# Kernel optimization log

Measured on AMD Instinct MI355X. Metric: run time of the kernel, lower is better.

Reference implementation:

```python
import jax, jax.numpy as jnp
import numpy as np

NUM_ITER = 3
HEADS = 8
EPS = 1e-8

def _ln(x, g, b, eps=1e-5):
    mu = x.mean(-1, keepdims=True)
    var = ((x - mu) ** 2).mean(-1, keepdims=True)
    return (x - mu) * jax.lax.rsqrt(var + eps) * g + b

def setup_inputs() -> dict:
    key = jax.random.key(0)
    ks = jax.random.split(key, 10)
    B, Nkv, Din = 32, 4096, 256
    Nq, S, Hm = 16, 256, 512
    def xav(k, shape):
        lim = (6.0 / (shape[0] + shape[1])) ** 0.5
        return jax.random.uniform(k, shape, minval=-lim, maxval=lim, dtype=jnp.float32)
    return {
        "slots": jax.random.normal(ks[0], (Nq, S), dtype=jnp.float32),
        "inputs": jax.random.normal(ks[1], (B, Nkv, Din), dtype=jnp.float32),
        "norm_in_g": jnp.ones((Din,), jnp.float32), "norm_in_b": jnp.zeros((Din,), jnp.float32),
        "norm_slots_g": jnp.ones((S,), jnp.float32), "norm_slots_b": jnp.zeros((S,), jnp.float32),
        "norm_mlp_g": jnp.ones((S,), jnp.float32), "norm_mlp_b": jnp.zeros((S,), jnp.float32),
        "Wq": xav(ks[2], (S, S)), "Wk": xav(ks[3], (S, Din)), "Wv": xav(ks[4], (S, Din)),
        "gru_wih": xav(ks[5], (3 * S, S)),
        "gru_whh": jax.random.normal(ks[6], (3 * S, S), dtype=jnp.float32) * (1.0 / S ** 0.5),
        "gru_bih": jnp.zeros((3 * S,), jnp.float32), "gru_bhh": jnp.zeros((3 * S,), jnp.float32),
        "mlp_w1": xav(ks[7], (Hm, S)), "mlp_b1": jnp.zeros((Hm,), jnp.float32),
        "mlp_w2": xav(ks[8], (S, Hm)), "mlp_b2": jnp.zeros((S,), jnp.float32),
    }

def reference(slots, inputs, norm_in_g, norm_in_b, norm_slots_g, norm_slots_b,
              norm_mlp_g, norm_mlp_b, Wq, Wk, Wv, gru_wih, gru_whh, gru_bih, gru_bhh,
              mlp_w1, mlp_b1, mlp_w2, mlp_b2):
    B, Nkv, Din = inputs.shape
    Nq, S = slots.shape
    H = HEADS
    hd = S // H
    slots = jnp.broadcast_to(slots, (B, Nq, S))
    x = _ln(inputs, norm_in_g, norm_in_b)
    k = (x @ Wk.T).reshape(B, Nkv, H, hd).transpose(0, 2, 1, 3) * (hd ** -0.5)  # [B,H,Nkv,hd]
    v = (x @ Wv.T).reshape(B, Nkv, H, hd).transpose(0, 2, 1, 3)
    attn_vis = None
    for _ in range(NUM_ITER):
        slots_prev = slots
        s = _ln(slots, norm_slots_g, norm_slots_b)
        q = (s @ Wq.T).reshape(B, Nq, H, hd).transpose(0, 2, 1, 3)  # [B,H,Nq,hd]
        # logits [B,Nkv,H*Nq]; softmax jointly over heads and slots per key (slot-axis softmax)
        logits = jnp.einsum('bhkd,bhqd->bkhq', k, q).reshape(B, Nkv, H * Nq)
        attn = jax.nn.softmax(logits, axis=-1).reshape(B, Nkv, H, Nq).transpose(0, 2, 1, 3)  # [B,H,Nkv,Nq]
        attn_vis = attn.sum(1)  # [B,Nkv,Nq]
        attn_n = attn / (attn.sum(axis=2, keepdims=True) + EPS)  # normalize over keys
        updates = jnp.einsum('bhkq,bhkd->bqhd', attn_n, v).reshape(B, Nq, S)
        # GRUCell: gates order r,z,n
        xg = updates.reshape(-1, S)
        h = slots_prev.reshape(-1, S)
        gi = xg @ gru_wih.T + gru_bih
        gh = h @ gru_whh.T + gru_bhh
        ir, iz, inn = jnp.split(gi, 3, axis=-1)
        hr, hz, hn = jnp.split(gh, 3, axis=-1)
        r = jax.nn.sigmoid(ir + hr)
        z = jax.nn.sigmoid(iz + hz)
        n = jnp.tanh(inn + r * hn)
        slots = ((1.0 - z) * n + z * h).reshape(B, Nq, S)
        m = _ln(slots, norm_mlp_g, norm_mlp_b)
        slots = slots + (jax.nn.relu(m @ mlp_w1.T + mlp_b1) @ mlp_w2.T + mlp_b2)
    return (slots, attn_vis)
```

## Files before the change

### kernel.cpp

```cpp
#include <hip/hip_runtime.h>
#include <stdint.h>

typedef unsigned short u16;
typedef __attribute__((ext_vector_type(8))) _Float16 half8;
typedef __attribute__((ext_vector_type(4))) _Float16 half4;
typedef __attribute__((ext_vector_type(4))) float floatx4;

__device__ inline float bflo(unsigned u){ return __uint_as_float(u << 16); }
__device__ inline float bfhi(unsigned u){ return __uint_as_float(u & 0xffff0000u); }
__device__ inline float bf1(u16 v){ return __uint_as_float(((unsigned)v) << 16); }
__device__ inline u16 f2bf(float f){
  unsigned u = __float_as_uint(f);
  u += 0x7fffu + ((u >> 16) & 1u);
  return (u16)(u >> 16);
}
__device__ inline float dot8(uint4 w, float4 a, float4 b, float acc){
  acc = fmaf(bflo(w.x), a.x, acc); acc = fmaf(bfhi(w.x), a.y, acc);
  acc = fmaf(bflo(w.y), a.z, acc); acc = fmaf(bfhi(w.y), a.w, acc);
  acc = fmaf(bflo(w.z), b.x, acc); acc = fmaf(bfhi(w.z), b.y, acc);
  acc = fmaf(bflo(w.w), b.z, acc); acc = fmaf(bfhi(w.w), b.w, acc);
  return acc;
}

#define CW_SLOTS 0
#define CW_GIN   4096
#define CW_BIN   4352
#define CW_GS    4608
#define CW_BS    4864
#define CW_GM    5120
#define CW_BM    5376
#define CW_WQ    5632
#define CW_WK    71168
#define CW_WV    136704
#define CW_WIH   202240
#define CW_WHH   398848
#define CW_BIH   595456
#define CW_BHH   596224
#define CW_W1    596992
#define CW_B1    728064
#define CW_W2    728576
#define CW_B2    859648
#define CW_TOTAL 859904

__global__ void k_flag(const u16* __restrict__ probe, int* __restrict__ flag){
  int t = threadIdx.x;
  int bad = 0;
  #pragma unroll
  for (int i = 0; i < 4; i++){
    float x = bf1(probe[t + i * 256]);
    if (!(fabsf(x) < 1e6f)) bad = 1;
  }
  __shared__ int s;
  if (t == 0) s = 0;
  __syncthreads();
  if (bad) atomicOr(&s, 1);
  __syncthreads();
  if (t == 0) *flag = s;
}

struct CanonArgs { const void* p[18]; };

__global__ void k_canon(CanonArgs a, const int* __restrict__ flag, u16* __restrict__ cw){
  const int off[19] = {CW_SLOTS, CW_GIN, CW_BIN, CW_GS, CW_BS, CW_GM, CW_BM, CW_WQ,
                       CW_WK, CW_WV, CW_WIH, CW_WHH, CW_BIH, CW_BHH, CW_W1, CW_B1,
                       CW_W2, CW_B2, CW_TOTAL};
  int i = blockIdx.x * 256 + threadIdx.x;
  if (i >= CW_TOTAL) return;
  int f32m = *flag;
  int j = 0;
  while (i >= off[j + 1]) j++;
  int local = i - off[j];
  float v = f32m ? ((const float*)a.p[j])[local] : bf1(((const u16*)a.p[j])[local]);
  cw[i] = f2bf(v);
}

__global__ void k_init(const u16* __restrict__ cw, float* __restrict__ slots,
                       _Float16* __restrict__ wkvh)
{
  int idx = blockIdx.x * 256 + threadIdx.x;
  if (idx < 131072){
    float g = bf1(cw[CW_GIN + (idx & 255)]);
    wkvh[idx] = (_Float16)(bf1(cw[CW_WK + idx]) * g);
  } else {
    int i = idx - 131072;
    int d = i & 255;
    int q = (i >> 8) & 15;
    slots[i] = bf1(cw[CW_SLOTS + q * 256 + d]);
  }
}

__global__ void k_beta(const u16* __restrict__ cw, float* __restrict__ beta){
  int c = blockIdx.x * 256 + threadIdx.x;
  if (c >= 512) return;
  float a = 0.f;
  for (int d = 0; d < 256; d++)
    a = fmaf(bf1(cw[CW_BIN + d]), bf1(cw[CW_WK + c * 256 + d]), a);
  beta[c] = a;
}

__global__ __launch_bounds__(256) void k0_stats(
    const void* __restrict__ inp, const int* __restrict__ flag, float2* __restrict__ stats)
{
  int f32m = *flag;
  int g = blockIdx.x * 256 + threadIdx.x;
  int row = g >> 4, l = g & 15;
  float sum = 0.f, sq = 0.f;
  if (f32m){
    const float* rp = (const float*)inp + row * 256 + l * 16;
    #pragma unroll
    for (int i = 0; i < 4; i++){
      float4 v = ((const float4*)rp)[i];
      sum += v.x + v.y + v.z + v.w;
      sq = fmaf(v.x, v.x, sq); sq = fmaf(v.y, v.y, sq);
      sq = fmaf(v.z, v.z, sq); sq = fmaf(v.w, v.w, sq);
    }
  } else {
    const u16* rp = (const u16*)inp + row * 256 + l * 16;
    #pragma unroll
    for (int i = 0; i < 2; i++){
      uint4 u = ((const uint4*)rp)[i];
      unsigned w[4] = {u.x, u.y, u.z, u.w};
      #pragma unroll
      for (int p = 0; p < 4; p++){
        float a = bflo(w[p]), b = bfhi(w[p]);
        sum += a + b; sq = fmaf(a, a, sq); sq = fmaf(b, b, sq);
      }
    }
  }
  #pragma unroll
  for (int m = 1; m < 16; m <<= 1){ sum += __shfl_xor(sum, m); sq += __shfl_xor(sq, m); }
  if (l == 0){
    float mu = sum * (1.f/256.f);
    float var = sq * (1.f/256.f) - mu * mu;
    stats[row] = make_float2(mu, rsqrtf(var + 1e-5f));
  }
}

__global__ __launch_bounds__(256) void k1_gemm(
    const void* __restrict__ inp, const int* __restrict__ flag,
    const float2* __restrict__ stats, const float* __restrict__ beta,
    const _Float16* __restrict__ wkvh, _Float16* __restrict__ kh, _Float16* __restrict__ vT)
{
  int f32m = *flag;
  int tid = threadIdx.x;
  int wv = tid >> 6, lane = tid & 63;
  int m16 = lane & 15, q4 = lane >> 4;
  int nb = blockIdx.y;
  long rowb0 = (long)blockIdx.x * 128;
  int colW = nb * 256 + wv * 64;

  half8 bfr[4][8];
  #pragma unroll
  for (int nt = 0; nt < 4; nt++)
    #pragma unroll
    for (int s = 0; s < 8; s++)
      bfr[nt][s] = *(const half8*)(wkvh + (colW + nt * 16 + m16) * 256 + s * 32 + q4 * 8);

  float bet[4];
  #pragma unroll
  for (int nt = 0; nt < 4; nt++) bet[nt] = beta[colW + nt * 16 + m16];

  for (int rt = 0; rt < 8; rt++){
    long rowb = rowb0 + rt * 16;
    long myRow = rowb + m16;
    float2 st = stats[myRow];
    float mu = st.x, rstd = st.y;

    half8 af[8];
    if (f32m){
      const float* rp = (const float*)inp + myRow * 256 + q4 * 8;
      #pragma unroll
      for (int s = 0; s < 8; s++){
        float4 x0 = *(const float4*)(rp + s * 32);
        float4 x1 = *(const float4*)(rp + s * 32 + 4);
        af[s][0] = (_Float16)((x0.x - mu) * rstd); af[s][1] = (_Float16)((x0.y - mu) * rstd);
        af[s][2] = (_Float16)((x0.z - mu) * rstd); af[s][3] = (_Float16)((x0.w - mu) * rstd);
        af[s][4] = (_Float16)((x1.x - mu) * rstd); af[s][5] = (_Float16)((x1.y - mu) * rstd);
        af[s][6] = (_Float16)((x1.z - mu) * rstd); af[s][7] = (_Float16)((x1.w - mu) * rstd);
      }
    } else {
      const u16* rp = (const u16*)inp + myRow * 256 + q4 * 8;
      #pragma unroll
      for (int s = 0; s < 8; s++){
        uint4 xu = *(const uint4*)(rp + s * 32);
        unsigned xw[4] = {xu.x, xu.y, xu.z, xu.w};
        #pragma unroll
        for (int p = 0; p < 4; p++){
          af[s][2*p]   = (_Float16)((bflo(xw[p]) - mu) * rstd);
          af[s][2*p+1] = (_Float16)((bfhi(xw[p]) - mu) * rstd);
        }
      }
    }

    floatx4 acc[4];
    #pragma unroll
    for (int nt = 0; nt < 4; nt++){
      acc[nt][0] = bet[nt]; acc[nt][1] = bet[nt]; acc[nt][2] = bet[nt]; acc[nt][3] = bet[nt];
    }
    #pragma unroll
    for (int s = 0; s < 8; s++)
      #pragma unroll
      for (int nt = 0; nt < 4; nt++)
        acc[nt] = __builtin_amdgcn_mfma_f32_16x16x32_f16(af[s], bfr[nt][s], acc[nt], 0, 0, 0);

    if (nb == 0){
      long crow = rowb + q4 * 4;
      #pragma unroll
      for (int nt = 0; nt < 4; nt++)
        #pragma unroll
        for (int r = 0; r < 4; r++)
          kh[(crow + r) * 256 + colW + nt * 16 + m16] = (_Float16)acc[nt][r];
    } else {
      int b = (int)(rowb >> 12);
      int key = ((int)rowb & 4095) + q4 * 4;
      int kg  = key >> 6;
      int klo = key & 63;
      #pragma unroll
      for (int nt = 0; nt < 4; nt++){
        int cv = (colW - 256) + nt * 16 + m16;
        half4 pk;
        pk[0] = (_Float16)acc[nt][0]; pk[1] = (_Float16)acc[nt][1];
        pk[2] = (_Float16)acc[nt][2]; pk[3] = (_Float16)acc[nt][3];
        *(half4*)(vT + (((long)b * 64 + kg) * 256 + cv) * 64 + klo) = pk;
      }
    }
  }
}

__global__ __launch_bounds__(256) void k2_q(
    const float* __restrict__ slots, const u16* __restrict__ cw, _Float16* __restrict__ qh,
    float* __restrict__ denom, float* __restrict__ numer, int lastIter)
{
  const u16* gq = cw + CW_GS;
  const u16* bq = cw + CW_BS;
  const u16* Wq = cw + CW_WQ;
  int row = blockIdx.x, tid = threadIdx.x;
  if (lastIter) numer[row * 256 + tid] = 0.f;
  if (row < 16) denom[row * 256 + tid] = 0.f;
  int wv = tid >> 6, lane = tid & 63;
  float x = slots[row * 256 + tid];
  float s = x, s2 = x * x;
  #pragma unroll
  for (int m = 1; m < 64; m <<= 1){ s += __shfl_xor(s, m); s2 += __shfl_xor(s2, m); }
  __shared__ float red[8];
  if (lane == 0){ red[wv] = s; red[4 + wv] = s2; }
  __syncthreads();
  float tot  = red[0] + red[1] + red[2] + red[3];
  float tot2 = red[4] + red[5] + red[6] + red[7];
  float mu = tot * (1.f/256.f);
  float rstd = rsqrtf(tot2 * (1.f/256.f) - mu * mu + 1e-5f);
  __shared__ float sln[256];
  sln[tid] = (x - mu) * rstd * bf1(gq[tid]) + bf1(bq[tid]);
  __syncthreads();
  const u16* wr = Wq + tid * 256;
  float a = 0.f;
  for (int k = 0; k < 256; k += 8){
    uint4 wu = *(const uint4*)(wr + k);
    float4 l0 = *(const float4*)(sln + k);
    float4 l1 = *(const float4*)(sln + k + 4);
    a = dot8(wu, l0, l1, a);
  }
  qh[row * 256 + tid] = (_Float16)(a * 0.17677669529663687f);
}

__global__ __launch_bounds__(256) void k3_attn(
    const _Float16* __restrict__ kh, const _Float16* __restrict__ vT,
    const _Float16* __restrict__ qh,
    float* __restrict__ denom, float* __restrict__ numer,
    void* __restrict__ out_scratch, const int* __restrict__ flag, int lastIter)
{
  int f32m = *flag;
  int tid = threadIdx.x;
  int wv = tid >> 6, lane = tid & 63;
  int m16 = lane & 15, q4 = lane >> 4;
  int b = blockIdx.x, chunk = blockIdx.y;
  __shared__ float lds_l[64 * 129];

  half8 qf[2];
  #pragma unroll
  for (int hh = 0; hh < 2; hh++){
    int h = wv * 2 + hh;
    qf[hh] = *(const half8*)(qh + (b * 16 + m16) * 256 + h * 32 + q4 * 8);
  }
  float pd[2] = {0.f, 0.f};
  floatx4 un[2][2];
  #pragma unroll
  for (int hh = 0; hh < 2; hh++)
    #pragma unroll
    for (int dt = 0; dt < 2; dt++) un[hh][dt] = (floatx4)0.f;

  half8 afp[4][2];
  {
    int key0 = chunk * 256;
    #pragma unroll
    for (int sub = 0; sub < 4; sub++){
      long rowb = (long)b * 4096 + key0 + sub * 16;
      #pragma unroll
      for (int hh = 0; hh < 2; hh++)
        afp[sub][hh] = *(const half8*)(kh + (rowb + m16) * 256 + (wv * 2 + hh) * 32 + q4 * 8);
    }
  }

  floatx4 z4 = (floatx4)0.f;
  for (int grp = 0; grp < 4; grp++){
    int key0 = chunk * 256 + grp * 64;
    #pragma unroll
    for (int sub = 0; sub < 4; sub++){
      #pragma unroll
      for (int hh = 0; hh < 2; hh++){
        int h = wv * 2 + hh;
        floatx4 d = __builtin_amdgcn_mfma_f32_16x16x32_f16(afp[sub][hh], qf[hh], z4, 0, 0, 0);
        #pragma unroll
        for (int r = 0; r < 4; r++)
          lds_l[(sub * 16 + q4 * 4 + r) * 129 + h * 16 + m16] = d[r];
      }
    }
    if (grp < 3){
      int keyn = key0 + 64;
      #pragma unroll
      for (int sub = 0; sub < 4; sub++){
        long rowb = (long)b * 4096 + keyn + sub * 16;
        #pragma unroll
        for (int hh = 0; hh < 2; hh++)
          afp[sub][hh] = *(const half8*)(kh + (rowb + m16) * 256 + (wv * 2 + hh) * 32 + q4 * 8);
      }
    }
    __syncthreads();
    half8 vfr[2][2][2];
    {
      int kg = key0 >> 6;
      #pragma unroll
      for (int ks = 0; ks < 2; ks++)
        #pragma unroll
        for (int hh = 0; hh < 2; hh++)
          #pragma unroll
          for (int dt = 0; dt < 2; dt++)
            vfr[ks][hh][dt] = *(const half8*)(vT +
                (((long)b * 64 + kg) * 256 + (wv * 2 + hh) * 32 + dt * 16 + m16) * 64
                + ks * 32 + q4 * 8);
    }
    {
      int qq = tid & 15;
      #pragma unroll
      for (int half_ = 0; half_ < 4; half_++){
        int kk = (tid >> 4) + half_ * 16;
        float l[8];
        #pragma unroll
        for (int h8 = 0; h8 < 8; h8++) l[h8] = lds_l[kk * 129 + h8 * 16 + qq];
        float M = l[0];
        #pragma unroll
        for (int h8 = 1; h8 < 8; h8++) M = fmaxf(M, l[h8]);
        #pragma unroll
        for (int msk = 1; msk < 16; msk <<= 1) M = fmaxf(M, __shfl_xor(M, msk));
        float p[8], sl = 0.f;
        #pragma unroll
        for (int h8 = 0; h8 < 8; h8++){ p[h8] = __expf(l[h8] - M); sl += p[h8]; }
        float St = sl;
        #pragma unroll
        for (int msk = 1; msk < 16; msk <<= 1) St += __shfl_xor(St, msk);
        float rS = 1.f / St;
        if (lastIter){
          float av = sl * rS;
          long idx = 131072 + ((long)b * 4096 + key0 + kk) * 16 + qq;
          if (f32m) ((float*)out_scratch)[idx] = av;
          else      ((u16*)out_scratch)[idx]   = f2bf(av);
        }
        #pragma unroll
        for (int h8 = 0; h8 < 8; h8++) lds_l[kk * 129 + h8 * 16 + qq] = p[h8] * rS;
      }
    }
    __syncthreads();
    #pragma unroll
    for (int hh = 0; hh < 2; hh++){
      int h = wv * 2 + hh;
      #pragma unroll
      for (int ks = 0; ks < 2; ks++){
        float pv[8];
        #pragma unroll
        for (int j = 0; j < 8; j++) pv[j] = lds_l[(ks * 32 + q4 * 8 + j) * 129 + h * 16 + m16];
        float ps = 0.f;
        #pragma unroll
        for (int j = 0; j < 8; j++) ps += pv[j];
        pd[hh] += ps;
        half8 bfr;
        #pragma unroll
        for (int j = 0; j < 8; j++) bfr[j] = (_Float16)pv[j];
        #pragma unroll
        for (int dt = 0; dt < 2; dt++)
          un[hh][dt] = __builtin_amdgcn_mfma_f32_16x16x32_f16(vfr[ks][hh][dt], bfr, un[hh][dt], 0, 0, 0);
      }
    }
    __syncthreads();
  }
  _Float16* pp = (_Float16*)((u16*)out_scratch + (f32m ? 262144 : 131072))
                 + (long)chunk * 131072;
  #pragma unroll
  for (int hh = 0; hh < 2; hh++){
    int h = wv * 2 + hh;
    float t = pd[hh];
    t += __shfl_xor(t, 16); t += __shfl_xor(t, 32);
    if (q4 == 0) atomicAdd(&denom[(b * 8 + h) * 16 + m16], t);
    if (lastIter){
      #pragma unroll
      for (int dt = 0; dt < 2; dt++)
        #pragma unroll
        for (int r = 0; r < 4; r++)
          atomicAdd(&numer[((b * 8 + h) * 16 + m16) * 32 + dt * 16 + q4 * 4 + r], un[hh][dt][r]);
    } else {
      #pragma unroll
      for (int dt = 0; dt < 2; dt++){
        half4 st;
        #pragma unroll
        for (int r = 0; r < 4; r++) st[r] = (_Float16)un[hh][dt][r];
        *(half4*)(pp + ((b * 8 + h) * 16 + m16) * 32 + dt * 16 + q4 * 4) = st;
      }
    }
  }
}

__global__ void k_reduce(const void* __restrict__ out_scratch, const int* __restrict__ flag,
                         float* __restrict__ numer){
  int i = blockIdx.x * 256 + threadIdx.x;
  int f32m = *flag;
  const _Float16* pp = (const _Float16*)((const u16*)out_scratch + (f32m ? 262144 : 131072));
  float s = 0.f;
  #pragma unroll
  for (int c = 0; c < 16; c++) s += (float)pp[(long)c * 131072 + i];
  numer[i] = s;
}

__global__ __launch_bounds__(256) void k4a_gru(
    const float* __restrict__ slots, const float* __restrict__ numer, const float* __restrict__ denom,
    const u16* __restrict__ cw, float* __restrict__ mid)
{
  const u16* wih = cw + CW_WIH;
  const u16* whh = cw + CW_WHH;
  const u16* bih = cw + CW_BIH;
  const u16* bhh = cw + CW_BHH;
  int jc = blockIdx.x, rg = blockIdx.y;
  int tid = threadIdx.x;
  __shared__ float u_s[8][256];
  __shared__ float h_s[8][256];
  {
    int hh = tid >> 5, dh = tid & 31;
    for (int i = 0; i < 8; i++){
      int row = rg * 8 + i;
      int b = row >> 4, slot = row & 15;
      float den = denom[(b * 8 + hh) * 16 + slot] + 1e-8f;
      u_s[i][tid] = numer[((b * 8 + hh) * 16 + slot) * 32 + dh] / den;
      h_s[i][tid] = slots[row * 256 + tid];
    }
  }
  __syncthreads();
  int rl = tid >> 5, jl = tid & 31;
  int j = jc * 32 + jl;
  int row = rg * 8 + rl;
  const u16* wir = wih + j * 256;
  const u16* wiz = wih + (256 + j) * 256;
  const u16* win = wih + (512 + j) * 256;
  const u16* whr = whh + j * 256;
  const u16* whz = whh + (256 + j) * 256;
  const u16* whn = whh + (512 + j) * 256;
  float air = 0, aiz = 0, ain = 0, ahr = 0, ahz = 0, ahn = 0;
  for (int k = 0; k < 256; k += 8){
    float4 u0 = *(const float4*)(&u_s[rl][k]);
    float4 u1 = *(const float4*)(&u_s[rl][k + 4]);
    float4 h0 = *(const float4*)(&h_s[rl][k]);
    float4 h1 = *(const float4*)(&h_s[rl][k + 4]);
    air = dot8(*(const uint4*)(wir + k), u0, u1, air);
    aiz = dot8(*(const uint4*)(wiz + k), u0, u1, aiz);
    ain = dot8(*(const uint4*)(win + k), u0, u1, ain);
    ahr = dot8(*(const uint4*)(whr + k), h0, h1, ahr);
    ahz = dot8(*(const uint4*)(whz + k), h0, h1, ahz);
    ahn = dot8(*(const uint4*)(whn + k), h0, h1, ahn);
  }
  float gr = air + bf1(bih[j])       + ahr + bf1(bhh[j]);
  float gz = aiz + bf1(bih[256 + j]) + ahz + bf1(bhh[256 + j]);
  float r = 1.f / (1.f + __expf(-gr));
  float z = 1.f / (1.f + __expf(-gz));
  float nn = tanhf(ain + bf1(bih[512 + j]) + r * (ahn + bf1(bhh[512 + j])));
  float h = h_s[rl][j];
  mid[row * 256 + j] = (1.f - z) * nn + z * h;
}

__global__ __launch_bounds__(256) void k4b_mlp(
    const float* __restrict__ mid, const u16* __restrict__ cw,
    float* __restrict__ slots, void* __restrict__ out_base,
    const int* __restrict__ flag, int lastIter)
{
  int f32m = *flag;
  const u16* gm = cw + CW_GM;
  const u16* bm = cw + CW_BM;
  const u16* w1 = cw + CW_W1;
  const u16* b1 = cw + CW_B1;
  const u16* w2 = cw + CW_W2;
  const u16* b2 = cw + CW_B2;
  int row = blockIdx.x, tid = threadIdx.x;
  int wv = tid >> 6, lane = tid & 63;
  float x = mid[row * 256 + tid];
  float s = x, s2 = x * x;
  #pragma unroll
  for (int m = 1; m < 64; m <<= 1){ s += __shfl_xor(s, m); s2 += __shfl_xor(s2, m); }
  __shared__ float red[8];
  if (lane == 0){ red[wv] = s; red[4 + wv] = s2; }
  __syncthreads();
  float tot  = red[0] + red[1] + red[2] + red[3];
  float tot2 = red[4] + red[5] + red[6] + red[7];
  float mu = tot * (1.f/256.f);
  float rstd = rsqrtf(tot2 * (1.f/256.f) - mu * mu + 1e-5f);
  __shared__ float ls[256];
  __shared__ float h1[512];
  ls[tid] = (x - mu) * rstd * bf1(gm[tid]) + bf1(bm[tid]);
  __syncthreads();
  const u16* w1a = w1 + tid * 256;
  const u16* w1b = w1 + (tid + 256) * 256;
  float a0 = 0.f, a1 = 0.f;
  for (int k = 0; k < 256; k += 8){
    float4 l0 = *(const float4*)(ls + k);
    float4 l1 = *(const float4*)(ls + k + 4);
    a0 = dot8(*(const uint4*)(w1a + k), l0, l1, a0);
    a1 = dot8(*(const uint4*)(w1b + k), l0, l1, a1);
  }
  h1[tid]       = fmaxf(a0 + bf1(b1[tid]), 0.f);
  h1[tid + 256] = fmaxf(a1 + bf1(b1[tid + 256]), 0.f);
  __syncthreads();
  const u16* w2r = w2 + tid * 512;
  float a = 0.f;
  for (int k = 0; k < 512; k += 8){
    float4 l0 = *(const float4*)(h1 + k);
    float4 l1 = *(const float4*)(h1 + k + 4);
    a = dot8(*(const uint4*)(w2r + k), l0, l1, a);
  }
  float res = x + a + bf1(b2[tid]);
  slots[row * 256 + tid] = res;
  if (lastIter){
    int idx = row * 256 + tid;
    if (f32m) ((float*)out_base)[idx] = res;
    else      ((u16*)out_base)[idx]   = f2bf(res);
  }
}

extern "C" void kernel_launch(void* const* d_in, const int* in_sizes, int n_in,
                              void* d_out, int out_size, void* d_ws, size_t ws_size,
                              hipStream_t stream)
{
  char* ws = (char*)d_ws;
  int*  flagp    = (int*)ws;
  u16*  cw       = (u16*)(ws + 256);
  _Float16* qh   = (_Float16*)(ws + 1720064);
  _Float16* wkvh = (_Float16*)(ws + 1982208);
  float* slots   = (float*)(ws + 2244352);
  float* mid     = (float*)(ws + 2768640);
  float* numer   = (float*)(ws + 3292928);
  float* denom   = (float*)(ws + 3817216);
  _Float16* kh   = (_Float16*)(ws + 3833600);
  _Float16* vT   = (_Float16*)(ws + 70942464);
  float2* stats  = (float2*)(ws + 2768640);
  float*  beta   = (float*)(ws + 3817216);

  CanonArgs ca;
  ca.p[0]  = d_in[0];   ca.p[1]  = d_in[2];   ca.p[2]  = d_in[3];
  ca.p[3]  = d_in[4];   ca.p[4]  = d_in[5];   ca.p[5]  = d_in[6];
  ca.p[6]  = d_in[7];   ca.p[7]  = d_in[8];   ca.p[8]  = d_in[9];
  ca.p[9]  = d_in[10];  ca.p[10] = d_in[11];  ca.p[11] = d_in[12];
  ca.p[12] = d_in[13];  ca.p[13] = d_in[14];  ca.p[14] = d_in[15];
  ca.p[15] = d_in[16];  ca.p[16] = d_in[17];  ca.p[17] = d_in[18];

  k_flag<<<1, 256, 0, stream>>>((const u16*)d_in[1], flagp);
  k_canon<<<(CW_TOTAL + 255) / 256, 256, 0, stream>>>(ca, flagp, cw);
  k_init<<<1024, 256, 0, stream>>>(cw, slots, wkvh);
  k_beta<<<2, 256, 0, stream>>>(cw, beta);
  k0_stats<<<8192, 256, 0, stream>>>(d_in[1], flagp, stats);
  k1_gemm<<<dim3(1024, 2), 256, 0, stream>>>(d_in[1], flagp, stats, beta, wkvh, kh, vT);
  for (int it = 0; it < 3; it++){
    int last = (it == 2) ? 1 : 0;
    k2_q<<<512, 256, 0, stream>>>(slots, cw, qh, denom, numer, last);
    k3_attn<<<dim3(32, 16), 256, 0, stream>>>(kh, vT, qh, denom, numer, d_out, flagp, last);
    if (!last) k_reduce<<<512, 256, 0, stream>>>(d_out, flagp, numer);
    k4a_gru<<<dim3(8, 64), 256, 0, stream>>>(slots, numer, denom, cw, mid);
    k4b_mlp<<<512, 256, 0, stream>>>(mid, cw, slots, d_out, flagp, last);
  }
}
```

Baseline: 789.2 us.

## Fuse LayerNorm stats into projection GEMM and fold partial reduction into GRU

Removes the separate input-statistics kernel. The GEMM now multiplies raw inputs and computes each row's mean and rstd in-register, then applies the normalization afterwards as rstd*(acc - mu*colsum) + beta, using a precomputed gamma-weighted column sum of Wk. It also removes the k_reduce kernel by summing the 16 fp16 partial numerators inside the GRU kernel's shared-memory load, and adds a launch-bounds occupancy hint to the GEMM. The aim is to avoid a second full read of the 32x4096x256 input and two kernel launches. In exchange, raw unnormalized inputs are cast to fp16, which can cost precision, and every GRU block redundantly re-sums the partials.

```diff
diff --git a/kernel.cpp b/kernel.cpp
--- a/kernel.cpp
+++ b/kernel.cpp
@@ -89,56 +89,23 @@
   }
 }
 
-__global__ void k_beta(const u16* __restrict__ cw, float* __restrict__ beta){
+__global__ void k_beta(const u16* __restrict__ cw, float* __restrict__ beta,
+                       float* __restrict__ colsum){
   int c = blockIdx.x * 256 + threadIdx.x;
   if (c >= 512) return;
-  float a = 0.f;
-  for (int d = 0; d < 256; d++)
-    a = fmaf(bf1(cw[CW_BIN + d]), bf1(cw[CW_WK + c * 256 + d]), a);
+  float a = 0.f, s = 0.f;
+  for (int d = 0; d < 256; d++){
+    float w = bf1(cw[CW_WK + c * 256 + d]);
+    a = fmaf(bf1(cw[CW_BIN + d]), w, a);
+    s = fmaf(bf1(cw[CW_GIN + d]), w, s);
+  }
   beta[c] = a;
-}
-
-__global__ __launch_bounds__(256) void k0_stats(
-    const void* __restrict__ inp, const int* __restrict__ flag, float2* __restrict__ stats)
-{
-  int f32m = *flag;
-  int g = blockIdx.x * 256 + threadIdx.x;
-  int row = g >> 4, l = g & 15;
-  float sum = 0.f, sq = 0.f;
-  if (f32m){
-    const float* rp = (const float*)inp + row * 256 + l * 16;
-    #pragma unroll
-    for (int i = 0; i < 4; i++){
-      float4 v = ((const float4*)rp)[i];
-      sum += v.x + v.y + v.z + v.w;
-      sq = fmaf(v.x, v.x, sq); sq = fmaf(v.y, v.y, sq);
-      sq = fmaf(v.z, v.z, sq); sq = fmaf(v.w, v.w, sq);
-    }
-  } else {
-    const u16* rp = (const u16*)inp + row * 256 + l * 16;
-    #pragma unroll
-    for (int i = 0; i < 2; i++){
-      uint4 u = ((const uint4*)rp)[i];
-      unsigned w[4] = {u.x, u.y, u.z, u.w};
-      #pragma unroll
-      for (int p = 0; p < 4; p++){
-        float a = bflo(w[p]), b = bfhi(w[p]);
-        sum += a + b; sq = fmaf(a, a, sq); sq = fmaf(b, b, sq);
-      }
-    }
-  }
-  #pragma unroll
-  for (int m = 1; m < 16; m <<= 1){ sum += __shfl_xor(sum, m); sq += __shfl_xor(sq, m); }
-  if (l == 0){
-    float mu = sum * (1.f/256.f);
-    float var = sq * (1.f/256.f) - mu * mu;
-    stats[row] = make_float2(mu, rsqrtf(var + 1e-5f));
-  }
-}
-
-__global__ __launch_bounds__(256) void k1_gemm(
+  colsum[c] = s;
+}
+
+__global__ __launch_bounds__(256, 4) void k1_gemm(
     const void* __restrict__ inp, const int* __restrict__ flag,
-    const float2* __restrict__ stats, const float* __restrict__ beta,
+    const float* __restrict__ beta, const float* __restrict__ colsum,
     const _Float16* __restrict__ wkvh, _Float16* __restrict__ kh, _Float16* __restrict__ vT)
 {
   int f32m = *flag;
@@ -156,16 +123,18 @@
     for (int s = 0; s < 8; s++)
       bfr[nt][s] = *(const half8*)(wkvh + (colW + nt * 16 + m16) * 256 + s * 32 + q4 * 8);
 
-  float bet[4];
-  #pragma unroll
-  for (int nt = 0; nt < 4; nt++) bet[nt] = beta[colW + nt * 16 + m16];
+  float bet[4], cs[4];
+  #pragma unroll
+  for (int nt = 0; nt < 4; nt++){
+    bet[nt] = beta[colW + nt * 16 + m16];
+    cs[nt]  = colsum[colW + nt * 16 + m16];
+  }
 
   for (int rt = 0; rt < 8; rt++){
     long rowb = rowb0 + rt * 16;
     long myRow = rowb + m16;
-    float2 st = stats[myRow];
-    float mu = st.x, rstd = st.y;
-
+
+    float sum = 0.f, sq = 0.f;
     half8 af[8];
     if (f32m){
       const float* rp = (const float*)inp + myRow * 256 + q4 * 8;
@@ -173,10 +142,15 @@
       for (int s = 0; s < 8; s++){
         float4 x0 = *(const float4*)(rp + s * 32);
         float4 x1 = *(const float4*)(rp + s * 32 + 4);
-        af[s][0] = (_Float16)((x0.x - mu) * rstd); af[s][1] = (_Float16)((x0.y - mu) * rstd);
-        af[s][2] = (_Float16)((x0.z - mu) * rstd); af[s][3] = (_Float16)((x0.w - mu) * rstd);
-        af[s][4] = (_Float16)((x1.x - mu) * rstd); af[s][5] = (_Float16)((x1.y - mu) * rstd);
-        af[s][6] = (_Float16)((x1.z - mu) * rstd); af[s][7] = (_Float16)((x1.w - mu) * rstd);
+        sum += x0.x + x0.y + x0.z + x0.w + x1.x + x1.y + x1.z + x1.w;
+        sq = fmaf(x0.x, x0.x, sq); sq = fmaf(x0.y, x0.y, sq);
+        sq = fmaf(x0.z, x0.z, sq); sq = fmaf(x0.w, x0.w, sq);
+        sq = fmaf(x1.x, x1.x, sq); sq = fmaf(x1.y, x1.y, sq);
+        sq = fmaf(x1.z, x1.z, sq); sq = fmaf(x1.w, x1.w, sq);
+        af[s][0] = (_Float16)x0.x; af[s][1] = (_Float16)x0.y;
+        af[s][2] = (_Float16)x0.z; af[s][3] = (_Float16)x0.w;
+        af[s][4] = (_Float16)x1.x; af[s][5] = (_Float16)x1.y;
+        af[s][6] = (_Float16)x1.z; af[s][7] = (_Float16)x1.w;
       }
     } else {
       const u16* rp = (const u16*)inp + myRow * 256 + q4 * 8;
@@ -186,22 +160,38 @@
         unsigned xw[4] = {xu.x, xu.y, xu.z, xu.w};
         #pragma unroll
         for (int p = 0; p < 4; p++){
-          af[s][2*p]   = (_Float16)((bflo(xw[p]) - mu) * rstd);
-          af[s][2*p+1] = (_Float16)((bfhi(xw[p]) - mu) * rstd);
+          float a = bflo(xw[p]), b = bfhi(xw[p]);
+          sum += a + b; sq = fmaf(a, a, sq); sq = fmaf(b, b, sq);
+          af[s][2*p]   = (_Float16)a;
+          af[s][2*p+1] = (_Float16)b;
         }
       }
     }
+    sum += __shfl_xor(sum, 16); sq += __shfl_xor(sq, 16);
+    sum += __shfl_xor(sum, 32); sq += __shfl_xor(sq, 32);
+    float mu = sum * (1.f/256.f);
+    float rstd = rsqrtf(fmaf(-mu, mu, sq * (1.f/256.f)) + 1e-5f);
 
     floatx4 acc[4];
     #pragma unroll
-    for (int nt = 0; nt < 4; nt++){
-      acc[nt][0] = bet[nt]; acc[nt][1] = bet[nt]; acc[nt][2] = bet[nt]; acc[nt][3] = bet[nt];
-    }
+    for (int nt = 0; nt < 4; nt++) acc[nt] = (floatx4)0.f;
     #pragma unroll
     for (int s = 0; s < 8; s++)
       #pragma unroll
       for (int nt = 0; nt < 4; nt++)
         acc[nt] = __builtin_amdgcn_mfma_f32_16x16x32_f16(af[s], bfr[nt][s], acc[nt], 0, 0, 0);
+
+    float mur[4], rsr[4];
+    #pragma unroll
+    for (int r = 0; r < 4; r++){
+      mur[r] = __shfl(mu,   q4 * 4 + r);
+      rsr[r] = __shfl(rstd, q4 * 4 + r);
+    }
+    #pragma unroll
+    for (int nt = 0; nt < 4; nt++)
+      #pragma unroll
+      for (int r = 0; r < 4; r++)
+        acc[nt][r] = fmaf(rsr[r], fmaf(-mur[r], cs[nt], acc[nt][r]), bet[nt]);
 
     if (nb == 0){
       long crow = rowb + q4 * 4;
@@ -418,20 +408,10 @@
   }
 }
 
-__global__ void k_reduce(const void* __restrict__ out_scratch, const int* __restrict__ flag,
-                         float* __restrict__ numer){
-  int i = blockIdx.x * 256 + threadIdx.x;
-  int f32m = *flag;
-  const _Float16* pp = (const _Float16*)((const u16*)out_scratch + (f32m ? 262144 : 131072));
-  float s = 0.f;
-  #pragma unroll
-  for (int c = 0; c < 16; c++) s += (float)pp[(long)c * 131072 + i];
-  numer[i] = s;
-}
-
 __global__ __launch_bounds__(256) void k4a_gru(
     const float* __restrict__ slots, const float* __restrict__ numer, const float* __restrict__ denom,
-    const u16* __restrict__ cw, float* __restrict__ mid)
+    const u16* __restrict__ cw, float* __restrict__ mid,
+    const void* __restrict__ out_scratch, const int* __restrict__ flag, int lastIter)
 {
   const u16* wih = cw + CW_WIH;
   const u16* whh = cw + CW_WHH;
@@ -443,11 +423,22 @@
   __shared__ float h_s[8][256];
   {
     int hh = tid >> 5, dh = tid & 31;
+    const _Float16* pp = (const _Float16*)((const u16*)out_scratch
+                          + (*flag ? 262144 : 131072));
     for (int i = 0; i < 8; i++){
       int row = rg * 8 + i;
       int b = row >> 4, slot = row & 15;
+      int idx = ((b * 8 + hh) * 16 + slot) * 32 + dh;
       float den = denom[(b * 8 + hh) * 16 + slot] + 1e-8f;
-      u_s[i][tid] = numer[((b * 8 + hh) * 16 + slot) * 32 + dh] / den;
+      float nm;
+      if (lastIter){
+        nm = numer[idx];
+      } else {
+        nm = 0.f;
+        #pragma unroll
+        for (int c = 0; c < 16; c++) nm += (float)pp[(long)c * 131072 + idx];
+      }
+      u_s[i][tid] = nm / den;
       h_s[i][tid] = slots[row * 256 + tid];
     }
   }
@@ -555,8 +546,8 @@
   float* denom   = (float*)(ws + 3817216);
   _Float16* kh   = (_Float16*)(ws + 3833600);
   _Float16* vT   = (_Float16*)(ws + 70942464);
-  float2* stats  = (float2*)(ws + 2768640);
   float*  beta   = (float*)(ws + 3817216);
+  float*  colsum = beta + 512;
 
   CanonArgs ca;
   ca.p[0]  = d_in[0];   ca.p[1]  = d_in[2];   ca.p[2]  = d_in[3];
@@ -569,15 +560,13 @@
   k_flag<<<1, 256, 0, stream>>>((const u16*)d_in[1], flagp);
   k_canon<<<(CW_TOTAL + 255) / 256, 256, 0, stream>>>(ca, flagp, cw);
   k_init<<<1024, 256, 0, stream>>>(cw, slots, wkvh);
-  k_beta<<<2, 256, 0, stream>>>(cw, beta);
-  k0_stats<<<8192, 256, 0, stream>>>(d_in[1], flagp, stats);
-  k1_gemm<<<dim3(1024, 2), 256, 0, stream>>>(d_in[1], flagp, stats, beta, wkvh, kh, vT);
+  k_beta<<<2, 256, 0, stream>>>(cw, beta, colsum);
+  k1_gemm<<<dim3(1024, 2), 256, 0, stream>>>(d_in[1], flagp, beta, colsum, wkvh, kh, vT);
   for (int it = 0; it < 3; it++){
     int last = (it == 2) ? 1 : 0;
     k2_q<<<512, 256, 0, stream>>>(slots, cw, qh, denom, numer, last);
     k3_attn<<<dim3(32, 16), 256, 0, stream>>>(kh, vT, qh, denom, numer, d_out, flagp, last);
-    if (!last) k_reduce<<<512, 256, 0, stream>>>(d_out, flagp, numer);
-    k4a_gru<<<dim3(8, 64), 256, 0, stream>>>(slots, numer, denom, cw, mid);
+    k4a_gru<<<dim3(8, 64), 256, 0, stream>>>(slots, numer, denom, cw, mid, d_out, flagp, last);
     k4b_mlp<<<512, 256, 0, stream>>>(mid, cw, slots, d_out, flagp, last);
   }
 }
```

After: 1.037 ms. +31.4%, slower.
